# Kernel optimization log

Hardware: AMD Instinct MI355X
Metric: run time of the kernel (lower is better)

## Reference

```python
import jax, jax.numpy as jnp
import numpy as np

N_NODES = 50000
N_EDGES = 800000
N_REL = 3
N_GRAPHS = 500
EMB = 128
IN_DIM = EMB * 3
HID = 256
N_CLASS = 10
N_SHAPE, N_COLOR, MAX_POS = 8, 8, 128


def rgcn_layer(h, src, dst, etype, W, root, b):
    """PyG RGCNConv with default aggr='mean':
    out[v] = sum_r mean_{(j->v) in E_r} h[j] @ W[r] + h[v] @ root + b
    Aggregate raw features per (dst, relation) bucket, then apply relation matmuls.
    """
    N, R = h.shape[0], W.shape[0]
    seg = dst * R + etype  # combined (node, relation) segment id
    sums = jax.ops.segment_sum(h[src], seg, num_segments=N * R)          # (N*R, d)
    cnt = jax.ops.segment_sum(jnp.ones(seg.shape, h.dtype), seg, num_segments=N * R)
    mean = (sums / jnp.maximum(cnt, 1.0)[:, None]).reshape(N, R, -1)     # (N, R, d)
    return jnp.einsum('nrd,rdh->nh', mean, W) + h @ root + b


def setup_inputs() -> dict:
    key = jax.random.key(0)
    ks = jax.random.split(key, 20)
    f32 = jnp.float32
    inp = {
        's': jax.random.randint(ks[0], (N_NODES,), 0, N_SHAPE),
        'c': jax.random.randint(ks[1], (N_NODES,), 0, N_COLOR),
        'p': jax.random.randint(ks[2], (N_NODES,), 0, MAX_POS),
        'edge_index': jax.random.randint(ks[3], (2, N_EDGES), 0, N_NODES),
        'edge_type': jax.random.randint(ks[4], (N_EDGES,), 0, N_REL),
        'batch': jnp.sort(jax.random.randint(ks[5], (N_NODES,), 0, N_GRAPHS)),
        'shape_emb': jax.random.normal(ks[6], (N_SHAPE, EMB), f32),
        'color_emb': jax.random.normal(ks[7], (N_COLOR, EMB), f32),
        'pos_emb': jax.random.normal(ks[8], (MAX_POS, EMB), f32),
        'W1': jax.random.normal(ks[9], (N_REL, IN_DIM, HID), f32) / np.sqrt(IN_DIM),
        'root1': jax.random.normal(ks[10], (IN_DIM, HID), f32) / np.sqrt(IN_DIM),
        'b1': jnp.zeros((HID,), f32),
        'W2': jax.random.normal(ks[11], (N_REL, HID, HID), f32) / np.sqrt(HID),
        'root2': jax.random.normal(ks[12], (HID, HID), f32) / np.sqrt(HID),
        'b2': jnp.zeros((HID,), f32),
        'lin_w': jax.random.normal(ks[13], (HID, N_CLASS), f32) / np.sqrt(HID),
        'lin_b': jnp.zeros((N_CLASS,), f32),
    }
    return inp


def reference(s, c, p, edge_index, edge_type, batch,
              shape_emb, color_emb, pos_emb,
              W1, root1, b1, W2, root2, b2, lin_w, lin_b):
    src, dst = edge_index[0], edge_index[1]
    h = jnp.concatenate([shape_emb[s], color_emb[c], pos_emb[p]], axis=-1)  # (N, 3*emb)
    h = jax.nn.relu(rgcn_layer(h, src, dst, edge_type, W1, root1, b1))
    h = jax.nn.relu(rgcn_layer(h, src, dst, edge_type, W2, root2, b2))
    # global_mean_pool over graphs
    gsum = jax.ops.segment_sum(h, batch, num_segments=N_GRAPHS)
    gcnt = jax.ops.segment_sum(jnp.ones((h.shape[0],), h.dtype), batch, num_segments=N_GRAPHS)
    pooled = gsum / jnp.maximum(gcnt, 1.0)[:, None]
    return pooled @ lin_w + lin_b
```

## Files before the change

kernel.cpp:

```cpp
#include <hip/hip_runtime.h>
#include <hip/hip_bf16.h>

#define NN 50000
#define NE 800000
#define NR 3
#define NG 500
#define NB (NN * NR)
#define NCLS 10
#define NCMB 8192
#define CHUNK 2048
#define NBLK ((NB + CHUNK - 1) / CHUNK)

#define P1_COMBO   196
#define P1_ZCNT    586
#define P1_ZPOOL   502
#define P1_TAB     576
#define P1_WF      1024
#define P1_TOTAL   (P1_COMBO + P1_ZCNT + P1_ZPOOL + P1_TAB + P1_WF)
#define P2_CNT     3125
#define P2_COMB    (4 * NCMB)
#define P2_TOTAL   (P2_CNT + P2_COMB)

typedef __hip_bfloat16 bf16;
typedef __attribute__((ext_vector_type(8))) short short8;
typedef __attribute__((ext_vector_type(4))) float floatx4;

static __device__ __forceinline__ float b2f(bf16 x) { return __bfloat162float(x); }
static __device__ __forceinline__ bf16  f2b(float x) { return __float2bfloat16(x); }
static __device__ __forceinline__ float bs2f(short x) {
    return __bfloat162float(*reinterpret_cast<const bf16*>(&x));
}
static __device__ __forceinline__ short f2bs(float x) {
    bf16 b = __float2bfloat16(x);
    return *reinterpret_cast<const short*>(&b);
}

__global__ __launch_bounds__(256) void prep1(const int* __restrict__ s,
                                             const int* __restrict__ c,
                                             const int* __restrict__ p,
                                             const float* __restrict__ se,
                                             const float* __restrict__ ce,
                                             const float* __restrict__ pe,
                                             const float* __restrict__ W1,
                                             const float* __restrict__ root1,
                                             const float* __restrict__ W2,
                                             const float* __restrict__ root2,
                                             int* __restrict__ combo,
                                             unsigned* __restrict__ cnt,
                                             unsigned* __restrict__ poolz,
                                             float* __restrict__ tab,
                                             bf16* __restrict__ Wf) {
    int b = blockIdx.x, t = threadIdx.x;
    if (b < P1_COMBO) {
        int n = b * 256 + t;
        if (n < NN) combo[n] = (s[n] << 10) | (c[n] << 7) | p[n];
        return;
    }
    b -= P1_COMBO;
    if (b < P1_ZCNT) {
        int i = b * 256 + t;
        if (i < NB) cnt[i] = 0u;
        return;
    }
    b -= P1_ZCNT;
    if (b < P1_ZPOOL) {
        int i = b * 256 + t;
        if (i < NG * 256 + NG) poolz[i] = 0u;
        return;
    }
    b -= P1_ZPOOL;
    if (b < P1_TAB) {
        int r = b / 144, row = b % 144;
        const float* A; int segk;
        if (row < 8)       { A = se + row * 128;        segk = 0; }
        else if (row < 16) { A = ce + (row - 8) * 128;  segk = 128; }
        else               { A = pe + (row - 16) * 128; segk = 256; }
        const float* W = (r < 3) ? (W1 + (size_t)r * 384 * 256) : root1;
        float acc = 0.f;
        for (int k = 0; k < 128; ++k)
            acc += A[k] * W[(size_t)(segk + k) * 256 + t];
        tab[((size_t)r * 144 + row) * 256 + t] = acc;
        return;
    }
    b -= P1_TAB;
    {
        int idx = b * 256 + t;
        int j     = idx & 7;
        int lane  = (idx >> 3) & 63;
        int ni    = (idx >> 9) & 3;
        int chunk = (idx >> 11) & 31;
        int colblk = idx >> 16;
        int col = colblk * 64 + ni * 16 + (lane & 15);
        int k   = chunk * 32 + (lane >> 4) * 8 + j;
        float v = (k < 768) ? W2[((size_t)(k >> 8) * 256 + (k & 255)) * 256 + col]
                            : root2[(size_t)(k - 768) * 256 + col];
        Wf[idx] = f2b(v);
    }
}

__global__ __launch_bounds__(256) void prep2(const int* __restrict__ ei,
                                             const int* __restrict__ et,
                                             int* __restrict__ cnt,
                                             const float* __restrict__ tab,
                                             const float* __restrict__ b1,
                                             bf16* __restrict__ comb) {
    int b = blockIdx.x, t = threadIdx.x;
    if (b < P2_CNT) {
        int e = b * 256 + t;
        if (e < NE) atomicAdd(&cnt[ei[NE + e] * NR + et[e]], 1);
        return;
    }
    b -= P2_CNT;
    {
        int r = b >> 13, cmb = b & (NCMB - 1);
        int si = cmb >> 10, ci = (cmb >> 7) & 7, pi = cmb & 127;
        const float* tr = tab + (size_t)r * 144 * 256;
        float v = tr[si * 256 + t] + tr[(8 + ci) * 256 + t] + tr[(16 + pi) * 256 + t];
        if (r == 3) v += b1[t];
        comb[(size_t)b * 256 + t] = f2b(v);
    }
}

__global__ __launch_bounds__(256) void scan_block_sums(const int* __restrict__ cnt,
                                                       int* __restrict__ bsum) {
    __shared__ int sm[256];
    int b = blockIdx.x, t = threadIdx.x;
    int base = b * CHUNK + t * 8, s = 0;
#pragma unroll
    for (int j = 0; j < 8; ++j) { int i = base + j; if (i < NB) s += cnt[i]; }
    sm[t] = s; __syncthreads();
    for (int st = 128; st; st >>= 1) { if (t < st) sm[t] += sm[t + st]; __syncthreads(); }
    if (!t) bsum[b] = sm[0];
}

__global__ __launch_bounds__(256) void scan_write(const int* __restrict__ cnt,
                                                  const int* __restrict__ bsum,
                                                  int* __restrict__ off,
                                                  int* __restrict__ cursor) {
    int b = blockIdx.x, t = threadIdx.x;
    int bbase = 0;
    for (int i = 0; i < b; ++i) bbase += bsum[i];
    if (b == 0 && t == 0) {
        int tot = 0;
        for (int i = 0; i < NBLK; ++i) tot += bsum[i];
        off[NB] = tot;
    }
    int base = b * CHUNK + t * 8;
    int v[8], ts = 0;
#pragma unroll
    for (int j = 0; j < 8; ++j) { int i = base + j; v[j] = (i < NB) ? cnt[i] : 0; ts += v[j]; }
    int lane = t & 63, wv = t >> 6;
    int incl = ts;
    for (int d = 1; d < 64; d <<= 1) {
        int o = __shfl_up(incl, d, 64);
        if (lane >= d) incl += o;
    }
    __shared__ int wsum[4];
    if (lane == 63) wsum[wv] = incl;
    __syncthreads();
    int wbase = 0;
    for (int w = 0; w < wv; ++w) wbase += wsum[w];
    int run = bbase + wbase + incl - ts;
#pragma unroll
    for (int j = 0; j < 8; ++j) {
        int i = base + j;
        if (i < NB) { off[i] = run; cursor[i] = run; }
        run += v[j];
    }
}

__global__ __launch_bounds__(256) void scatter_edges(const int* __restrict__ ei,
                                                     const int* __restrict__ et,
                                                     const int* __restrict__ combo,
                                                     int* __restrict__ cursor,
                                                     int* __restrict__ eidx,
                                                     int* __restrict__ ecmb) {
    int e = blockIdx.x * 256 + threadIdx.x;
    if (e >= NE) return;
    int b = ei[NE + e] * NR + et[e];
    int pos = atomicAdd(&cursor[b], 1);
    int s = ei[e];
    eidx[pos] = s;
    ecmb[pos] = combo[s];
}

__global__ __launch_bounds__(256) void l1_fused(const int* __restrict__ off,
                                                const int* __restrict__ ecmb,
                                                const int* __restrict__ combo,
                                                const bf16* __restrict__ comb,
                                                bf16* __restrict__ h1) {
    int wave = threadIdx.x >> 6, lane = threadIdx.x & 63;
    int dst = blockIdx.x * 4 + wave;
    if (dst >= NN) return;
    int half = lane >> 5, li8 = (lane & 31) * 8;
    float acc[8];
    if (half == 0) {
        int cmbD = combo[dst];
        short8 rv = *(const short8*)(comb + ((size_t)(3 * NCMB) + cmbD) * 256 + li8);
#pragma unroll
        for (int i = 0; i < 8; ++i) acc[i] = bs2f(rv[i]);
    } else {
#pragma unroll
        for (int i = 0; i < 8; ++i) acc[i] = 0.f;
    }
    for (int r = 0; r < NR; ++r) {
        int lo = off[dst * NR + r], hi = off[dst * NR + r + 1];
        if (hi <= lo) continue;
        const bf16* cr = comb + (size_t)r * NCMB * 256;
        float s[8] = {};
        int j = lo;
        for (; j + 8 <= hi; j += 8) {
            int c0 = ecmb[j + half],     c1 = ecmb[j + 2 + half];
            int c2 = ecmb[j + 4 + half], c3 = ecmb[j + 6 + half];
            short8 v0 = *(const short8*)(cr + (size_t)c0 * 256 + li8);
            short8 v1 = *(const short8*)(cr + (size_t)c1 * 256 + li8);
            short8 v2 = *(const short8*)(cr + (size_t)c2 * 256 + li8);
            short8 v3 = *(const short8*)(cr + (size_t)c3 * 256 + li8);
#pragma unroll
            for (int i = 0; i < 8; ++i)
                s[i] += (bs2f(v0[i]) + bs2f(v1[i])) + (bs2f(v2[i]) + bs2f(v3[i]));
        }
        for (; j + 2 <= hi; j += 2) {
            int c0 = ecmb[j + half];
            short8 v0 = *(const short8*)(cr + (size_t)c0 * 256 + li8);
#pragma unroll
            for (int i = 0; i < 8; ++i) s[i] += bs2f(v0[i]);
        }
        if (j < hi && half == 0) {
            short8 v0 = *(const short8*)(cr + (size_t)ecmb[j] * 256 + li8);
#pragma unroll
            for (int i = 0; i < 8; ++i) s[i] += bs2f(v0[i]);
        }
        float inv = 1.0f / (float)(hi - lo);
#pragma unroll
        for (int i = 0; i < 8; ++i) {
            float tot = s[i] + __shfl_xor(s[i], 32);
            if (half == 0) acc[i] += tot * inv;
        }
    }
    if (half == 0) {
        short8 o;
#pragma unroll
        for (int i = 0; i < 8; ++i) o[i] = f2bs(fmaxf(acc[i], 0.f));
        *(short8*)(h1 + (size_t)dst * 256 + li8) = o;
    }
}

__global__ __launch_bounds__(256) void agg_all(const int* __restrict__ off,
                                               const int* __restrict__ eidx,
                                               const bf16* __restrict__ h1,
                                               bf16* __restrict__ hagg) {
    int wave = threadIdx.x >> 6, lane = threadIdx.x & 63;
    int dst = blockIdx.x * 4 + wave;
    if (dst >= NN) return;
    int half = lane >> 5, li8 = (lane & 31) * 8;
    for (int r = 0; r < NR; ++r) {
        int lo = off[dst * NR + r], hi = off[dst * NR + r + 1];
        float s[8] = {};
        int j = lo;
        for (; j + 8 <= hi; j += 8) {
            int e0 = eidx[j + half],     e1 = eidx[j + 2 + half];
            int e2 = eidx[j + 4 + half], e3 = eidx[j + 6 + half];
            short8 v0 = *(const short8*)(h1 + (size_t)e0 * 256 + li8);
            short8 v1 = *(const short8*)(h1 + (size_t)e1 * 256 + li8);
            short8 v2 = *(const short8*)(h1 + (size_t)e2 * 256 + li8);
            short8 v3 = *(const short8*)(h1 + (size_t)e3 * 256 + li8);
#pragma unroll
            for (int i = 0; i < 8; ++i)
                s[i] += (bs2f(v0[i]) + bs2f(v1[i])) + (bs2f(v2[i]) + bs2f(v3[i]));
        }
        for (; j + 2 <= hi; j += 2) {
            int e0 = eidx[j + half];
            short8 v0 = *(const short8*)(h1 + (size_t)e0 * 256 + li8);
#pragma unroll
            for (int i = 0; i < 8; ++i) s[i] += bs2f(v0[i]);
        }
        if (j < hi && half == 0) {
            short8 v0 = *(const short8*)(h1 + (size_t)eidx[j] * 256 + li8);
#pragma unroll
            for (int i = 0; i < 8; ++i) s[i] += bs2f(v0[i]);
        }
        float inv = (hi > lo) ? 1.0f / (float)(hi - lo) : 0.f;
        short8 o;
#pragma unroll
        for (int i = 0; i < 8; ++i) {
            float tot = s[i] + __shfl_xor(s[i], 32);
            o[i] = f2bs(tot * inv);
        }
        if (half == 0)
            *(short8*)(hagg + (size_t)dst * 768 + r * 256 + li8) = o;
    }
}

__global__ __launch_bounds__(256) void gemm_cat(const bf16* __restrict__ hagg,
                                                const bf16* __restrict__ h1,
                                                const bf16* __restrict__ Wf,
                                                const float* __restrict__ bias,
                                                const int* __restrict__ batch,
                                                float* __restrict__ pool,
                                                float* __restrict__ gcnt) {
    __shared__ short lds[4][2][32 * 40];
    const int t = threadIdx.x;
    const int wave = t >> 6, lane = t & 63;
    const int quad = lane >> 4, l16 = lane & 15;
    const int row0 = blockIdx.x * 32;
    const int colblk = wave;
    const int rsub = lane >> 2;
    const int ksub = (lane & 3) * 8;
    short* A0 = lds[wave][0];
    short* A1 = lds[wave][1];

    const int r0 = min(row0 + rsub, NN - 1);
    const int r1 = min(row0 + 16 + rsub, NN - 1);
    const bf16* gA0 = hagg + (size_t)r0 * 768 + ksub;
    const bf16* gA1 = hagg + (size_t)r1 * 768 + ksub;
    const bf16* gH0 = h1 + (size_t)r0 * 256 + ksub;
    const bf16* gH1 = h1 + (size_t)r1 * 256 + ksub;
    const short8* bbase = (const short8*)Wf + (size_t)colblk * 32 * 4 * 64 + lane;

    auto loadA2 = [&](int k0, short8& a0, short8& a1) {
        if (k0 < 768) { a0 = *(const short8*)(gA0 + k0); a1 = *(const short8*)(gA1 + k0); }
        else          { a0 = *(const short8*)(gH0 + k0 - 768); a1 = *(const short8*)(gH1 + k0 - 768); }
    };
    auto loadB = [&](int chunk, short8* bf4) {
        const short8* bp = bbase + (size_t)chunk * 4 * 64;
#pragma unroll
        for (int ni = 0; ni < 4; ++ni) bf4[ni] = bp[ni * 64];
    };

    floatx4 acc[2][4] = {};
    short8 aE0, aE1, bE[4];
    short8 aO0, aO1, bO[4];
    loadA2(0, aE0, aE1);  loadB(0, bE);
    loadA2(32, aO0, aO1); loadB(1, bO);

#pragma unroll
    for (int i = 0; i < 32; i += 2) {
        *(short8*)&A0[rsub * 40 + ksub] = aE0;
        *(short8*)&A0[(16 + rsub) * 40 + ksub] = aE1;
        {
            short8 af0 = *(const short8*)&A0[l16 * 40 + quad * 8];
            short8 af1 = *(const short8*)&A0[(16 + l16) * 40 + quad * 8];
#pragma unroll
            for (int ni = 0; ni < 4; ++ni) {
                acc[0][ni] = __builtin_amdgcn_mfma_f32_16x16x32_bf16(af0, bE[ni], acc[0][ni], 0, 0, 0);
                acc[1][ni] = __builtin_amdgcn_mfma_f32_16x16x32_bf16(af1, bE[ni], acc[1][ni], 0, 0, 0);
            }
        }
        if (i + 2 < 32) { loadA2((i + 2) * 32, aE0, aE1); loadB(i + 2, bE); }
        *(short8*)&A1[rsub * 40 + ksub] = aO0;
        *(short8*)&A1[(16 + rsub) * 40 + ksub] = aO1;
        {
            short8 af0 = *(const short8*)&A1[l16 * 40 + quad * 8];
            short8 af1 = *(const short8*)&A1[(16 + l16) * 40 + quad * 8];
#pragma unroll
            for (int ni = 0; ni < 4; ++ni) {
                acc[0][ni] = __builtin_amdgcn_mfma_f32_16x16x32_bf16(af0, bO[ni], acc[0][ni], 0, 0, 0);
                acc[1][ni] = __builtin_amdgcn_mfma_f32_16x16x32_bf16(af1, bO[ni], acc[1][ni], 0, 0, 0);
            }
        }
        if (i + 3 < 32) { loadA2((i + 3) * 32, aO0, aO1); loadB(i + 3, bO); }
    }

    __syncthreads();
    short* st = &lds[0][0][0];
#pragma unroll
    for (int mi = 0; mi < 2; ++mi) {
#pragma unroll
        for (int ni = 0; ni < 4; ++ni) {
            int n = colblk * 64 + ni * 16 + l16;
            float bn = bias[n];
#pragma unroll
            for (int ii = 0; ii < 4; ++ii) {
                int lrow = mi * 16 + quad * 4 + ii;
                float v = (row0 + lrow < NN) ? fmaxf(acc[mi][ni][ii] + bn, 0.f) : 0.f;
                st[lrow * 260 + n] = f2bs(v);
            }
        }
    }
    __syncthreads();
    int nrows = NN - row0; if (nrows > 32) nrows = 32;
    int curg = batch[row0];
    float a = 0.f, cntf = 0.f;
    for (int rr = 0; rr < nrows; ++rr) {
        int g = batch[row0 + rr];
        if (g != curg) {
            atomicAdd(&pool[(size_t)curg * 256 + t], a);
            if (t == 0) atomicAdd(&gcnt[curg], cntf);
            a = 0.f; cntf = 0.f; curg = g;
        }
        a += bs2f(st[rr * 260 + t]);
        cntf += 1.f;
    }
    atomicAdd(&pool[(size_t)curg * 256 + t], a);
    if (t == 0) atomicAdd(&gcnt[curg], cntf);
}

__global__ __launch_bounds__(256) void final_head(const float* __restrict__ pool,
                                                  const float* __restrict__ gcnt,
                                                  const float* __restrict__ lin_w,
                                                  const float* __restrict__ lin_b,
                                                  float* __restrict__ out) {
    __shared__ float sm[256];
    int g = blockIdx.x, t = threadIdx.x;
    float inv = 1.0f / fmaxf(gcnt[g], 1.0f);
    sm[t] = pool[(size_t)g * 256 + t] * inv;
    __syncthreads();
    if (t < NCLS) {
        float s = lin_b[t];
        for (int d = 0; d < 256; ++d) s += sm[d] * lin_w[d * NCLS + t];
        out[g * NCLS + t] = s;
    }
}

extern "C" void kernel_launch(void* const* d_in, const int* in_sizes, int n_in,
                              void* d_out, int out_size, void* d_ws, size_t ws_size,
                              hipStream_t stream) {
    const int*   s_idx = (const int*)d_in[0];
    const int*   c_idx = (const int*)d_in[1];
    const int*   p_idx = (const int*)d_in[2];
    const int*   ei    = (const int*)d_in[3];
    const int*   et    = (const int*)d_in[4];
    const int*   batch = (const int*)d_in[5];
    const float* se    = (const float*)d_in[6];
    const float* ce    = (const float*)d_in[7];
    const float* pe    = (const float*)d_in[8];
    const float* W1    = (const float*)d_in[9];
    const float* root1 = (const float*)d_in[10];
    const float* b1    = (const float*)d_in[11];
    const float* W2    = (const float*)d_in[12];
    const float* root2 = (const float*)d_in[13];
    const float* b2    = (const float*)d_in[14];
    const float* lin_w = (const float*)d_in[15];
    const float* lin_b = (const float*)d_in[16];
    float* out = (float*)d_out;

    char* w = (char*)d_ws;
    size_t o = 0;
    auto alloc = [&](size_t bytes) -> void* {
        o = (o + 15) & ~(size_t)15;
        void* ptr = w + o;
        o += bytes;
        return ptr;
    };
    bf16*  hagg   = (bf16*) alloc((size_t)NN * 768 * 2);
    bf16*  h1     = (bf16*) alloc((size_t)NN * 256 * 2);
    bf16*  comb   = (bf16*) alloc((size_t)4 * NCMB * 256 * 2);
    int*   combo  = (int*)  alloc((size_t)NN * 4);
    int*   eidx   = (int*)  alloc((size_t)NE * 4);
    int*   ecmb   = (int*)  alloc((size_t)NE * 4);
    int*   cnt    = (int*)  alloc((size_t)NB * 4);
    int*   off    = (int*)  alloc((size_t)(NB + 1) * 4);
    int*   cursor = (int*)  alloc((size_t)NB * 4);
    int*   bsum   = (int*)  alloc((size_t)NBLK * 4);
    float* tab    = (float*)alloc((size_t)4 * 144 * 256 * 4);
    bf16*  Wf     = (bf16*) alloc((size_t)256 * 1024 * 2);
    float* pool   = (float*)alloc((size_t)NG * 256 * 4);
    float* gcnt  = (float*)alloc((size_t)NG * 4);
    (void)ws_size;

    prep1<<<P1_TOTAL, 256, 0, stream>>>(s_idx, c_idx, p_idx, se, ce, pe,
                                        W1, root1, W2, root2,
                                        combo, (unsigned*)cnt, (unsigned*)pool, tab, Wf);
    prep2<<<P2_TOTAL, 256, 0, stream>>>(ei, et, cnt, tab, b1, comb);
    scan_block_sums<<<NBLK, 256, 0, stream>>>(cnt, bsum);
    scan_write<<<NBLK, 256, 0, stream>>>(cnt, bsum, off, cursor);
    scatter_edges<<<(NE + 255) / 256, 256, 0, stream>>>(ei, et, combo, cursor, eidx, ecmb);
    l1_fused<<<(NN + 3) / 4, 256, 0, stream>>>(off, ecmb, combo, comb, h1);
    agg_all<<<(NN + 3) / 4, 256, 0, stream>>>(off, eidx, h1, hagg);
    gemm_cat<<<(NN + 31) / 32, 256, 0, stream>>>(hagg, h1, Wf, b2, batch, pool, gcnt);
    final_head<<<NG, 256, 0, stream>>>(pool, gcnt, lin_w, lin_b, out);
}
```

Baseline: 395.0 us.

## Interleave three relation gathers per node and pack edge source/combo into int2

The two gather kernels now walk all three relation buckets of a destination node in one masked loop, so loads from each relation are in flight together instead of serialised per relation. Tail handling uses predicated loads with zero masks rather than separate remainder loops. The scatter step writes the source index and combo id as one int2, replacing two separate arrays. This adds wasted masked loads when bucket sizes are uneven, and each kernel now reads 8-byte entries where it used only 4 bytes.

```diff
diff --git a/kernel.cpp b/kernel.cpp
--- a/kernel.cpp
+++ b/kernel.cpp
@@ -173,19 +173,17 @@
                                                      const int* __restrict__ et,
                                                      const int* __restrict__ combo,
                                                      int* __restrict__ cursor,
-                                                     int* __restrict__ eidx,
-                                                     int* __restrict__ ecmb) {
+                                                     int2* __restrict__ esc) {
     int e = blockIdx.x * 256 + threadIdx.x;
     if (e >= NE) return;
     int b = ei[NE + e] * NR + et[e];
     int pos = atomicAdd(&cursor[b], 1);
     int s = ei[e];
-    eidx[pos] = s;
-    ecmb[pos] = combo[s];
+    esc[pos] = make_int2(s, combo[s]);
 }
 
 __global__ __launch_bounds__(256) void l1_fused(const int* __restrict__ off,
-                                                const int* __restrict__ ecmb,
+                                                const int2* __restrict__ esc,
                                                 const int* __restrict__ combo,
                                                 const bf16* __restrict__ comb,
                                                 bf16* __restrict__ h1) {
@@ -193,102 +191,106 @@
     int dst = blockIdx.x * 4 + wave;
     if (dst >= NN) return;
     int half = lane >> 5, li8 = (lane & 31) * 8;
-    float acc[8];
-    if (half == 0) {
-        int cmbD = combo[dst];
-        short8 rv = *(const short8*)(comb + ((size_t)(3 * NCMB) + cmbD) * 256 + li8);
-#pragma unroll
-        for (int i = 0; i < 8; ++i) acc[i] = bs2f(rv[i]);
-    } else {
-#pragma unroll
-        for (int i = 0; i < 8; ++i) acc[i] = 0.f;
-    }
-    for (int r = 0; r < NR; ++r) {
-        int lo = off[dst * NR + r], hi = off[dst * NR + r + 1];
-        if (hi <= lo) continue;
-        const bf16* cr = comb + (size_t)r * NCMB * 256;
-        float s[8] = {};
-        int j = lo;
-        for (; j + 8 <= hi; j += 8) {
-            int c0 = ecmb[j + half],     c1 = ecmb[j + 2 + half];
-            int c2 = ecmb[j + 4 + half], c3 = ecmb[j + 6 + half];
-            short8 v0 = *(const short8*)(cr + (size_t)c0 * 256 + li8);
-            short8 v1 = *(const short8*)(cr + (size_t)c1 * 256 + li8);
-            short8 v2 = *(const short8*)(cr + (size_t)c2 * 256 + li8);
-            short8 v3 = *(const short8*)(cr + (size_t)c3 * 256 + li8);
-#pragma unroll
-            for (int i = 0; i < 8; ++i)
-                s[i] += (bs2f(v0[i]) + bs2f(v1[i])) + (bs2f(v2[i]) + bs2f(v3[i]));
-        }
-        for (; j + 2 <= hi; j += 2) {
-            int c0 = ecmb[j + half];
-            short8 v0 = *(const short8*)(cr + (size_t)c0 * 256 + li8);
-#pragma unroll
-            for (int i = 0; i < 8; ++i) s[i] += bs2f(v0[i]);
-        }
-        if (j < hi && half == 0) {
-            short8 v0 = *(const short8*)(cr + (size_t)ecmb[j] * 256 + li8);
-#pragma unroll
-            for (int i = 0; i < 8; ++i) s[i] += bs2f(v0[i]);
-        }
-        float inv = 1.0f / (float)(hi - lo);
-#pragma unroll
-        for (int i = 0; i < 8; ++i) {
-            float tot = s[i] + __shfl_xor(s[i], 32);
-            if (half == 0) acc[i] += tot * inv;
-        }
-    }
-    if (half == 0) {
-        short8 o;
-#pragma unroll
-        for (int i = 0; i < 8; ++i) o[i] = f2bs(fmaxf(acc[i], 0.f));
+    int o0 = off[dst * NR],     o1 = off[dst * NR + 1],
+        o2 = off[dst * NR + 2], o3 = off[dst * NR + 3];
+    short8 rootv = {};
+    if (half == 0)
+        rootv = *(const short8*)(comb + ((size_t)(3 * NCMB) + combo[dst]) * 256 + li8);
+    const bf16* c0 = comb;
+    const bf16* c1 = comb + (size_t)NCMB * 256;
+    const bf16* c2 = comb + (size_t)2 * NCMB * 256;
+    float s0[8] = {}, s1[8] = {}, s2[8] = {};
+    int n = max((o1 - o0 + 1) >> 1, max((o2 - o1 + 1) >> 1, (o3 - o2 + 1) >> 1));
+    for (int k = 0; k < n; k += 2) {
+#pragma unroll
+        for (int kk = 0; kk < 2; ++kk) {
+            int i0 = o0 + 2 * (k + kk) + half;
+            int i1 = o1 + 2 * (k + kk) + half;
+            int i2 = o2 + 2 * (k + kk) + half;
+            bool g0 = i0 < o1, g1 = i1 < o2, g2 = i2 < o3;
+            int2 e0 = esc[g0 ? i0 : 0];
+            int2 e1 = esc[g1 ? i1 : 0];
+            int2 e2 = esc[g2 ? i2 : 0];
+            short8 v0 = *(const short8*)(c0 + (size_t)(g0 ? e0.y : 0) * 256 + li8);
+            short8 v1 = *(const short8*)(c1 + (size_t)(g1 ? e1.y : 0) * 256 + li8);
+            short8 v2 = *(const short8*)(c2 + (size_t)(g2 ? e2.y : 0) * 256 + li8);
+            float m0 = g0 ? 1.f : 0.f, m1 = g1 ? 1.f : 0.f, m2 = g2 ? 1.f : 0.f;
+#pragma unroll
+            for (int i = 0; i < 8; ++i) {
+                s0[i] += bs2f(v0[i]) * m0;
+                s1[i] += bs2f(v1[i]) * m1;
+                s2[i] += bs2f(v2[i]) * m2;
+            }
+        }
+    }
+    float inv0 = (o1 > o0) ? 1.f / (float)(o1 - o0) : 0.f;
+    float inv1 = (o2 > o1) ? 1.f / (float)(o2 - o1) : 0.f;
+    float inv2 = (o3 > o2) ? 1.f / (float)(o3 - o2) : 0.f;
+    short8 o;
+#pragma unroll
+    for (int i = 0; i < 8; ++i) {
+        float t0 = s0[i] + __shfl_xor(s0[i], 32);
+        float t1 = s1[i] + __shfl_xor(s1[i], 32);
+        float t2 = s2[i] + __shfl_xor(s2[i], 32);
+        float a = bs2f(rootv[i]) + t0 * inv0 + t1 * inv1 + t2 * inv2;
+        o[i] = f2bs(fmaxf(a, 0.f));
+    }
+    if (half == 0)
         *(short8*)(h1 + (size_t)dst * 256 + li8) = o;
-    }
 }
 
 __global__ __launch_bounds__(256) void agg_all(const int* __restrict__ off,
-                                               const int* __restrict__ eidx,
+                                               const int2* __restrict__ esc,
                                                const bf16* __restrict__ h1,
                                                bf16* __restrict__ hagg) {
     int wave = threadIdx.x >> 6, lane = threadIdx.x & 63;
     int dst = blockIdx.x * 4 + wave;
     if (dst >= NN) return;
     int half = lane >> 5, li8 = (lane & 31) * 8;
-    for (int r = 0; r < NR; ++r) {
-        int lo = off[dst * NR + r], hi = off[dst * NR + r + 1];
-        float s[8] = {};
-        int j = lo;
-        for (; j + 8 <= hi; j += 8) {
-            int e0 = eidx[j + half],     e1 = eidx[j + 2 + half];
-            int e2 = eidx[j + 4 + half], e3 = eidx[j + 6 + half];
-            short8 v0 = *(const short8*)(h1 + (size_t)e0 * 256 + li8);
-            short8 v1 = *(const short8*)(h1 + (size_t)e1 * 256 + li8);
-            short8 v2 = *(const short8*)(h1 + (size_t)e2 * 256 + li8);
-            short8 v3 = *(const short8*)(h1 + (size_t)e3 * 256 + li8);
-#pragma unroll
-            for (int i = 0; i < 8; ++i)
-                s[i] += (bs2f(v0[i]) + bs2f(v1[i])) + (bs2f(v2[i]) + bs2f(v3[i]));
-        }
-        for (; j + 2 <= hi; j += 2) {
-            int e0 = eidx[j + half];
-            short8 v0 = *(const short8*)(h1 + (size_t)e0 * 256 + li8);
-#pragma unroll
-            for (int i = 0; i < 8; ++i) s[i] += bs2f(v0[i]);
-        }
-        if (j < hi && half == 0) {
-            short8 v0 = *(const short8*)(h1 + (size_t)eidx[j] * 256 + li8);
-#pragma unroll
-            for (int i = 0; i < 8; ++i) s[i] += bs2f(v0[i]);
-        }
-        float inv = (hi > lo) ? 1.0f / (float)(hi - lo) : 0.f;
-        short8 o;
-#pragma unroll
-        for (int i = 0; i < 8; ++i) {
-            float tot = s[i] + __shfl_xor(s[i], 32);
-            o[i] = f2bs(tot * inv);
-        }
-        if (half == 0)
-            *(short8*)(hagg + (size_t)dst * 768 + r * 256 + li8) = o;
+    int o0 = off[dst * NR],     o1 = off[dst * NR + 1],
+        o2 = off[dst * NR + 2], o3 = off[dst * NR + 3];
+    float s0[8] = {}, s1[8] = {}, s2[8] = {};
+    int n = max((o1 - o0 + 1) >> 1, max((o2 - o1 + 1) >> 1, (o3 - o2 + 1) >> 1));
+    for (int k = 0; k < n; k += 2) {
+#pragma unroll
+        for (int kk = 0; kk < 2; ++kk) {
+            int i0 = o0 + 2 * (k + kk) + half;
+            int i1 = o1 + 2 * (k + kk) + half;
+            int i2 = o2 + 2 * (k + kk) + half;
+            bool g0 = i0 < o1, g1 = i1 < o2, g2 = i2 < o3;
+            int2 e0 = esc[g0 ? i0 : 0];
+            int2 e1 = esc[g1 ? i1 : 0];
+            int2 e2 = esc[g2 ? i2 : 0];
+            short8 v0 = *(const short8*)(h1 + (size_t)(g0 ? e0.x : 0) * 256 + li8);
+            short8 v1 = *(const short8*)(h1 + (size_t)(g1 ? e1.x : 0) * 256 + li8);
+            short8 v2 = *(const short8*)(h1 + (size_t)(g2 ? e2.x : 0) * 256 + li8);
+            float m0 = g0 ? 1.f : 0.f, m1 = g1 ? 1.f : 0.f, m2 = g2 ? 1.f : 0.f;
+#pragma unroll
+            for (int i = 0; i < 8; ++i) {
+                s0[i] += bs2f(v0[i]) * m0;
+                s1[i] += bs2f(v1[i]) * m1;
+                s2[i] += bs2f(v2[i]) * m2;
+            }
+        }
+    }
+    float inv0 = (o1 > o0) ? 1.f / (float)(o1 - o0) : 0.f;
+    float inv1 = (o2 > o1) ? 1.f / (float)(o2 - o1) : 0.f;
+    float inv2 = (o3 > o2) ? 1.f / (float)(o3 - o2) : 0.f;
+    short8 w0, w1, w2;
+#pragma unroll
+    for (int i = 0; i < 8; ++i) {
+        float t0 = s0[i] + __shfl_xor(s0[i], 32);
+        float t1 = s1[i] + __shfl_xor(s1[i], 32);
+        float t2 = s2[i] + __shfl_xor(s2[i], 32);
+        w0[i] = f2bs(t0 * inv0);
+        w1[i] = f2bs(t1 * inv1);
+        w2[i] = f2bs(t2 * inv2);
+    }
+    if (half == 0) {
+        bf16* hd = hagg + (size_t)dst * 768 + li8;
+        *(short8*)(hd)       = w0;
+        *(short8*)(hd + 256) = w1;
+        *(short8*)(hd + 512) = w2;
     }
 }
 
@@ -447,8 +449,7 @@
     bf16*  h1     = (bf16*) alloc((size_t)NN * 256 * 2);
     bf16*  comb   = (bf16*) alloc((size_t)4 * NCMB * 256 * 2);
     int*   combo  = (int*)  alloc((size_t)NN * 4);
-    int*   eidx   = (int*)  alloc((size_t)NE * 4);
-    int*   ecmb   = (int*)  alloc((size_t)NE * 4);
+    int2*  esc    = (int2*) alloc((size_t)NE * 8);
     int*   cnt    = (int*)  alloc((size_t)NB * 4);
     int*   off    = (int*)  alloc((size_t)(NB + 1) * 4);
     int*   cursor = (int*)  alloc((size_t)NB * 4);
@@ -465,9 +466,9 @@
     prep2<<<P2_TOTAL, 256, 0, stream>>>(ei, et, cnt, tab, b1, comb);
     scan_block_sums<<<NBLK, 256, 0, stream>>>(cnt, bsum);
     scan_write<<<NBLK, 256, 0, stream>>>(cnt, bsum, off, cursor);
-    scatter_edges<<<(NE + 255) / 256, 256, 0, stream>>>(ei, et, combo, cursor, eidx, ecmb);
-    l1_fused<<<(NN + 3) / 4, 256, 0, stream>>>(off, ecmb, combo, comb, h1);
-    agg_all<<<(NN + 3) / 4, 256, 0, stream>>>(off, eidx, h1, hagg);
+    scatter_edges<<<(NE + 255) / 256, 256, 0, stream>>>(ei, et, combo, cursor, esc);
+    l1_fused<<<(NN + 3) / 4, 256, 0, stream>>>(off, esc, combo, comb, h1);
+    agg_all<<<(NN + 3) / 4, 256, 0, stream>>>(off, esc, h1, hagg);
     gemm_cat<<<(NN + 31) / 32, 256, 0, stream>>>(hagg, h1, Wf, b2, batch, pool, gcnt);
     final_head<<<NG, 256, 0, stream>>>(pool, gcnt, lin_w, lin_b, out);
 }
```

Result: faster. 383.3 us (-2.9%).

## Fuse layer-2 aggregation into GEMM and pack edge src/combo into one word

Applied to the files above, without the earlier changes.

The layer-2 neighbor aggregation now runs inside the GEMM kernel. Each block gathers the mean-aggregated rows for its 32 nodes straight into a swizzled LDS tile, so the 150 MB-scale hagg intermediate is never written or re-read from global memory. The per-edge source index and combo index are packed into one 32-bit word, which halves the edge-list traffic. Layer 1 now walks all three relations in a single merged loop with per-edge weights. The trade-off is a large 64 KB LDS tile per block, which lowers occupancy, and the aggregation phase is serialized ahead of the MFMA phase within each block.

```diff
diff --git a/kernel.cpp b/kernel.cpp
--- a/kernel.cpp
+++ b/kernel.cpp
@@ -173,19 +173,17 @@
                                                      const int* __restrict__ et,
                                                      const int* __restrict__ combo,
                                                      int* __restrict__ cursor,
-                                                     int* __restrict__ eidx,
-                                                     int* __restrict__ ecmb) {
+                                                     unsigned* __restrict__ esc) {
     int e = blockIdx.x * 256 + threadIdx.x;
     if (e >= NE) return;
     int b = ei[NE + e] * NR + et[e];
     int pos = atomicAdd(&cursor[b], 1);
     int s = ei[e];
-    eidx[pos] = s;
-    ecmb[pos] = combo[s];
+    esc[pos] = ((unsigned)s << 13) | (unsigned)combo[s];
 }
 
 __global__ __launch_bounds__(256) void l1_fused(const int* __restrict__ off,
-                                                const int* __restrict__ ecmb,
+                                                const unsigned* __restrict__ esc,
                                                 const int* __restrict__ combo,
                                                 const bf16* __restrict__ comb,
                                                 bf16* __restrict__ h1) {
@@ -193,177 +191,178 @@
     int dst = blockIdx.x * 4 + wave;
     if (dst >= NN) return;
     int half = lane >> 5, li8 = (lane & 31) * 8;
-    float acc[8];
-    if (half == 0) {
-        int cmbD = combo[dst];
-        short8 rv = *(const short8*)(comb + ((size_t)(3 * NCMB) + cmbD) * 256 + li8);
-#pragma unroll
-        for (int i = 0; i < 8; ++i) acc[i] = bs2f(rv[i]);
-    } else {
-#pragma unroll
-        for (int i = 0; i < 8; ++i) acc[i] = 0.f;
-    }
-    for (int r = 0; r < NR; ++r) {
-        int lo = off[dst * NR + r], hi = off[dst * NR + r + 1];
-        if (hi <= lo) continue;
-        const bf16* cr = comb + (size_t)r * NCMB * 256;
-        float s[8] = {};
-        int j = lo;
-        for (; j + 8 <= hi; j += 8) {
-            int c0 = ecmb[j + half],     c1 = ecmb[j + 2 + half];
-            int c2 = ecmb[j + 4 + half], c3 = ecmb[j + 6 + half];
-            short8 v0 = *(const short8*)(cr + (size_t)c0 * 256 + li8);
-            short8 v1 = *(const short8*)(cr + (size_t)c1 * 256 + li8);
-            short8 v2 = *(const short8*)(cr + (size_t)c2 * 256 + li8);
-            short8 v3 = *(const short8*)(cr + (size_t)c3 * 256 + li8);
-#pragma unroll
-            for (int i = 0; i < 8; ++i)
-                s[i] += (bs2f(v0[i]) + bs2f(v1[i])) + (bs2f(v2[i]) + bs2f(v3[i]));
-        }
-        for (; j + 2 <= hi; j += 2) {
-            int c0 = ecmb[j + half];
-            short8 v0 = *(const short8*)(cr + (size_t)c0 * 256 + li8);
-#pragma unroll
-            for (int i = 0; i < 8; ++i) s[i] += bs2f(v0[i]);
-        }
-        if (j < hi && half == 0) {
-            short8 v0 = *(const short8*)(cr + (size_t)ecmb[j] * 256 + li8);
-#pragma unroll
-            for (int i = 0; i < 8; ++i) s[i] += bs2f(v0[i]);
-        }
-        float inv = 1.0f / (float)(hi - lo);
-#pragma unroll
-        for (int i = 0; i < 8; ++i) {
-            float tot = s[i] + __shfl_xor(s[i], 32);
-            if (half == 0) acc[i] += tot * inv;
-        }
-    }
-    if (half == 0) {
-        short8 o;
-#pragma unroll
-        for (int i = 0; i < 8; ++i) o[i] = f2bs(fmaxf(acc[i], 0.f));
+    int b0 = dst * NR;
+    int o0 = off[b0], o1 = off[b0 + 1], o2 = off[b0 + 2], o3 = off[b0 + 3];
+    float inv0 = (o1 > o0) ? 1.f / (float)(o1 - o0) : 0.f;
+    float inv1 = (o2 > o1) ? 1.f / (float)(o2 - o1) : 0.f;
+    float inv2 = (o3 > o2) ? 1.f / (float)(o3 - o2) : 0.f;
+    short8 rootv = {};
+    if (half == 0)
+        rootv = *(const short8*)(comb + ((size_t)(3 * NCMB) + combo[dst]) * 256 + li8);
+    float s[8] = {};
+    int j = o0;
+    for (; j + 8 <= o3; j += 8) {
+        int k0 = j + half, k1 = j + 2 + half, k2 = j + 4 + half, k3 = j + 6 + half;
+        unsigned e0 = esc[k0], e1 = esc[k1], e2 = esc[k2], e3 = esc[k3];
+        int ro0 = ((k0 >= o1) ? NCMB : 0) + ((k0 >= o2) ? NCMB : 0);
+        int ro1 = ((k1 >= o1) ? NCMB : 0) + ((k1 >= o2) ? NCMB : 0);
+        int ro2 = ((k2 >= o1) ? NCMB : 0) + ((k2 >= o2) ? NCMB : 0);
+        int ro3 = ((k3 >= o1) ? NCMB : 0) + ((k3 >= o2) ? NCMB : 0);
+        short8 v0 = *(const short8*)(comb + (size_t)(ro0 + (e0 & (NCMB - 1))) * 256 + li8);
+        short8 v1 = *(const short8*)(comb + (size_t)(ro1 + (e1 & (NCMB - 1))) * 256 + li8);
+        short8 v2 = *(const short8*)(comb + (size_t)(ro2 + (e2 & (NCMB - 1))) * 256 + li8);
+        short8 v3 = *(const short8*)(comb + (size_t)(ro3 + (e3 & (NCMB - 1))) * 256 + li8);
+        float w0 = (k0 >= o2) ? inv2 : ((k0 >= o1) ? inv1 : inv0);
+        float w1 = (k1 >= o2) ? inv2 : ((k1 >= o1) ? inv1 : inv0);
+        float w2 = (k2 >= o2) ? inv2 : ((k2 >= o1) ? inv1 : inv0);
+        float w3 = (k3 >= o2) ? inv2 : ((k3 >= o1) ? inv1 : inv0);
+#pragma unroll
+        for (int i = 0; i < 8; ++i)
+            s[i] += bs2f(v0[i]) * w0 + bs2f(v1[i]) * w1
+                  + bs2f(v2[i]) * w2 + bs2f(v3[i]) * w3;
+    }
+    for (; j + 2 <= o3; j += 2) {
+        int k0 = j + half;
+        unsigned e0 = esc[k0];
+        int ro0 = ((k0 >= o1) ? NCMB : 0) + ((k0 >= o2) ? NCMB : 0);
+        short8 v0 = *(const short8*)(comb + (size_t)(ro0 + (e0 & (NCMB - 1))) * 256 + li8);
+        float w0 = (k0 >= o2) ? inv2 : ((k0 >= o1) ? inv1 : inv0);
+#pragma unroll
+        for (int i = 0; i < 8; ++i) s[i] += bs2f(v0[i]) * w0;
+    }
+    if (j < o3 && half == 0) {
+        int k0 = j;
+        unsigned e0 = esc[k0];
+        int ro0 = ((k0 >= o1) ? NCMB : 0) + ((k0 >= o2) ? NCMB : 0);
+        short8 v0 = *(const short8*)(comb + (size_t)(ro0 + (e0 & (NCMB - 1))) * 256 + li8);
+        float w0 = (k0 >= o2) ? inv2 : ((k0 >= o1) ? inv1 : inv0);
+#pragma unroll
+        for (int i = 0; i < 8; ++i) s[i] += bs2f(v0[i]) * w0;
+    }
+    short8 o;
+#pragma unroll
+    for (int i = 0; i < 8; ++i) {
+        float tot = s[i] + __shfl_xor(s[i], 32);
+        o[i] = f2bs(fmaxf(bs2f(rootv[i]) + tot, 0.f));
+    }
+    if (half == 0)
         *(short8*)(h1 + (size_t)dst * 256 + li8) = o;
-    }
-}
-
-__global__ __launch_bounds__(256) void agg_all(const int* __restrict__ off,
-                                               const int* __restrict__ eidx,
-                                               const bf16* __restrict__ h1,
-                                               bf16* __restrict__ hagg) {
-    int wave = threadIdx.x >> 6, lane = threadIdx.x & 63;
-    int dst = blockIdx.x * 4 + wave;
-    if (dst >= NN) return;
-    int half = lane >> 5, li8 = (lane & 31) * 8;
-    for (int r = 0; r < NR; ++r) {
-        int lo = off[dst * NR + r], hi = off[dst * NR + r + 1];
-        float s[8] = {};
-        int j = lo;
-        for (; j + 8 <= hi; j += 8) {
-            int e0 = eidx[j + half],     e1 = eidx[j + 2 + half];
-            int e2 = eidx[j + 4 + half], e3 = eidx[j + 6 + half];
-            short8 v0 = *(const short8*)(h1 + (size_t)e0 * 256 + li8);
-            short8 v1 = *(const short8*)(h1 + (size_t)e1 * 256 + li8);
-            short8 v2 = *(const short8*)(h1 + (size_t)e2 * 256 + li8);
-            short8 v3 = *(const short8*)(h1 + (size_t)e3 * 256 + li8);
-#pragma unroll
-            for (int i = 0; i < 8; ++i)
-                s[i] += (bs2f(v0[i]) + bs2f(v1[i])) + (bs2f(v2[i]) + bs2f(v3[i]));
-        }
-        for (; j + 2 <= hi; j += 2) {
-            int e0 = eidx[j + half];
-            short8 v0 = *(const short8*)(h1 + (size_t)e0 * 256 + li8);
-#pragma unroll
-            for (int i = 0; i < 8; ++i) s[i] += bs2f(v0[i]);
-        }
-        if (j < hi && half == 0) {
-            short8 v0 = *(const short8*)(h1 + (size_t)eidx[j] * 256 + li8);
-#pragma unroll
-            for (int i = 0; i < 8; ++i) s[i] += bs2f(v0[i]);
-        }
-        float inv = (hi > lo) ? 1.0f / (float)(hi - lo) : 0.f;
-        short8 o;
-#pragma unroll
-        for (int i = 0; i < 8; ++i) {
-            float tot = s[i] + __shfl_xor(s[i], 32);
-            o[i] = f2bs(tot * inv);
-        }
-        if (half == 0)
-            *(short8*)(hagg + (size_t)dst * 768 + r * 256 + li8) = o;
-    }
-}
-
-__global__ __launch_bounds__(256) void gemm_cat(const bf16* __restrict__ hagg,
+}
+
+__global__ __launch_bounds__(256) void l2_fused(const int* __restrict__ off,
+                                                const unsigned* __restrict__ esc,
                                                 const bf16* __restrict__ h1,
                                                 const bf16* __restrict__ Wf,
                                                 const float* __restrict__ bias,
                                                 const int* __restrict__ batch,
                                                 float* __restrict__ pool,
                                                 float* __restrict__ gcnt) {
-    __shared__ short lds[4][2][32 * 40];
+    __shared__ short A[32 * 1024];
     const int t = threadIdx.x;
     const int wave = t >> 6, lane = t & 63;
+    const int half = lane >> 5, li8 = (lane & 31) * 8;
+    const int row0 = blockIdx.x * 32;
+
+    for (int d = 0; d < 8; ++d) {
+        int dstrow = wave * 8 + d;
+        int dst = row0 + dstrow;
+        bool val = dst < NN;
+        int b0 = val ? dst * NR : 0;
+        int o0 = off[b0], o1 = off[b0 + 1], o2 = off[b0 + 2], o3 = off[b0 + 3];
+        if (!val) { o1 = o0; o2 = o0; o3 = o0; }
+        int lo = o0;
+#pragma unroll
+        for (int r = 0; r < NR; ++r) {
+            int hi = (r == 0) ? o1 : (r == 1) ? o2 : o3;
+            float s[8] = {};
+            int j = lo;
+            for (; j + 8 <= hi; j += 8) {
+                unsigned e0 = esc[j + half],     e1 = esc[j + 2 + half];
+                unsigned e2 = esc[j + 4 + half], e3 = esc[j + 6 + half];
+                short8 v0 = *(const short8*)(h1 + (size_t)(e0 >> 13) * 256 + li8);
+                short8 v1 = *(const short8*)(h1 + (size_t)(e1 >> 13) * 256 + li8);
+                short8 v2 = *(const short8*)(h1 + (size_t)(e2 >> 13) * 256 + li8);
+                short8 v3 = *(const short8*)(h1 + (size_t)(e3 >> 13) * 256 + li8);
+#pragma unroll
+                for (int i = 0; i < 8; ++i)
+                    s[i] += (bs2f(v0[i]) + bs2f(v1[i])) + (bs2f(v2[i]) + bs2f(v3[i]));
+            }
+            for (; j + 2 <= hi; j += 2) {
+                unsigned e0 = esc[j + half];
+                short8 v0 = *(const short8*)(h1 + (size_t)(e0 >> 13) * 256 + li8);
+#pragma unroll
+                for (int i = 0; i < 8; ++i) s[i] += bs2f(v0[i]);
+            }
+            if (j < hi && half == 0) {
+                unsigned e0 = esc[j];
+                short8 v0 = *(const short8*)(h1 + (size_t)(e0 >> 13) * 256 + li8);
+#pragma unroll
+                for (int i = 0; i < 8; ++i) s[i] += bs2f(v0[i]);
+            }
+            float inv = (hi > lo) ? 1.f / (float)(hi - lo) : 0.f;
+            short8 o;
+#pragma unroll
+            for (int i = 0; i < 8; ++i) {
+                float tot = s[i] + __shfl_xor(s[i], 32);
+                o[i] = f2bs(tot * inv);
+            }
+            if (half == 0) {
+                int colb = (r * 256 + li8) * 2;
+                *(short8*)((char*)A + dstrow * 2048 + (colb ^ ((dstrow & 7) << 4))) = o;
+            }
+            lo = hi;
+        }
+        if (half == 0) {
+            short8 hv = {};
+            if (val) hv = *(const short8*)(h1 + (size_t)dst * 256 + li8);
+            int colb = (768 + li8) * 2;
+            *(short8*)((char*)A + dstrow * 2048 + (colb ^ ((dstrow & 7) << 4))) = hv;
+        }
+    }
+    __syncthreads();
+
     const int quad = lane >> 4, l16 = lane & 15;
-    const int row0 = blockIdx.x * 32;
     const int colblk = wave;
-    const int rsub = lane >> 2;
-    const int ksub = (lane & 3) * 8;
-    short* A0 = lds[wave][0];
-    short* A1 = lds[wave][1];
-
-    const int r0 = min(row0 + rsub, NN - 1);
-    const int r1 = min(row0 + 16 + rsub, NN - 1);
-    const bf16* gA0 = hagg + (size_t)r0 * 768 + ksub;
-    const bf16* gA1 = hagg + (size_t)r1 * 768 + ksub;
-    const bf16* gH0 = h1 + (size_t)r0 * 256 + ksub;
-    const bf16* gH1 = h1 + (size_t)r1 * 256 + ksub;
     const short8* bbase = (const short8*)Wf + (size_t)colblk * 32 * 4 * 64 + lane;
-
-    auto loadA2 = [&](int k0, short8& a0, short8& a1) {
-        if (k0 < 768) { a0 = *(const short8*)(gA0 + k0); a1 = *(const short8*)(gA1 + k0); }
-        else          { a0 = *(const short8*)(gH0 + k0 - 768); a1 = *(const short8*)(gH1 + k0 - 768); }
-    };
     auto loadB = [&](int chunk, short8* bf4) {
         const short8* bp = bbase + (size_t)chunk * 4 * 64;
 #pragma unroll
         for (int ni = 0; ni < 4; ++ni) bf4[ni] = bp[ni * 64];
     };
+    auto ldA = [&](int row, int colE) -> short8 {
+        int byte = (colE * 2) ^ ((row & 7) << 4);
+        return *(const short8*)((const char*)A + row * 2048 + byte);
+    };
 
     floatx4 acc[2][4] = {};
-    short8 aE0, aE1, bE[4];
-    short8 aO0, aO1, bO[4];
-    loadA2(0, aE0, aE1);  loadB(0, bE);
-    loadA2(32, aO0, aO1); loadB(1, bO);
-
-#pragma unroll
-    for (int i = 0; i < 32; i += 2) {
-        *(short8*)&A0[rsub * 40 + ksub] = aE0;
-        *(short8*)&A0[(16 + rsub) * 40 + ksub] = aE1;
+    short8 bE[4], bO[4];
+    loadB(0, bE); loadB(1, bO);
+#pragma unroll
+    for (int ch = 0; ch < 32; ch += 2) {
         {
-            short8 af0 = *(const short8*)&A0[l16 * 40 + quad * 8];
-            short8 af1 = *(const short8*)&A0[(16 + l16) * 40 + quad * 8];
+            short8 af0 = ldA(l16, ch * 32 + quad * 8);
+            short8 af1 = ldA(16 + l16, ch * 32 + quad * 8);
 #pragma unroll
             for (int ni = 0; ni < 4; ++ni) {
                 acc[0][ni] = __builtin_amdgcn_mfma_f32_16x16x32_bf16(af0, bE[ni], acc[0][ni], 0, 0, 0);
                 acc[1][ni] = __builtin_amdgcn_mfma_f32_16x16x32_bf16(af1, bE[ni], acc[1][ni], 0, 0, 0);
             }
         }
-        if (i + 2 < 32) { loadA2((i + 2) * 32, aE0, aE1); loadB(i + 2, bE); }
-        *(short8*)&A1[rsub * 40 + ksub] = aO0;
-        *(short8*)&A1[(16 + rsub) * 40 + ksub] = aO1;
+        if (ch + 2 < 32) loadB(ch + 2, bE);
         {
-            short8 af0 = *(const short8*)&A1[l16 * 40 + quad * 8];
-            short8 af1 = *(const short8*)&A1[(16 + l16) * 40 + quad * 8];
+            short8 af0 = ldA(l16, (ch + 1) * 32 + quad * 8);
+            short8 af1 = ldA(16 + l16, (ch + 1) * 32 + quad * 8);
 #pragma unroll
             for (int ni = 0; ni < 4; ++ni) {
                 acc[0][ni] = __builtin_amdgcn_mfma_f32_16x16x32_bf16(af0, bO[ni], acc[0][ni], 0, 0, 0);
                 acc[1][ni] = __builtin_amdgcn_mfma_f32_16x16x32_bf16(af1, bO[ni], acc[1][ni], 0, 0, 0);
             }
         }
-        if (i + 3 < 32) { loadA2((i + 3) * 32, aO0, aO1); loadB(i + 3, bO); }
+        if (ch + 3 < 32) loadB(ch + 3, bO);
     }
 
     __syncthreads();
-    short* st = &lds[0][0][0];
+    short* st = A;
 #pragma unroll
     for (int mi = 0; mi < 2; ++mi) {
 #pragma unroll
@@ -443,20 +442,18 @@
         o += bytes;
         return ptr;
     };
-    bf16*  hagg   = (bf16*) alloc((size_t)NN * 768 * 2);
-    bf16*  h1     = (bf16*) alloc((size_t)NN * 256 * 2);
-    bf16*  comb   = (bf16*) alloc((size_t)4 * NCMB * 256 * 2);
-    int*   combo  = (int*)  alloc((size_t)NN * 4);
-    int*   eidx   = (int*)  alloc((size_t)NE * 4);
-    int*   ecmb   = (int*)  alloc((size_t)NE * 4);
-    int*   cnt    = (int*)  alloc((size_t)NB * 4);
-    int*   off    = (int*)  alloc((size_t)(NB + 1) * 4);
-    int*   cursor = (int*)  alloc((size_t)NB * 4);
-    int*   bsum   = (int*)  alloc((size_t)NBLK * 4);
-    float* tab    = (float*)alloc((size_t)4 * 144 * 256 * 4);
-    bf16*  Wf     = (bf16*) alloc((size_t)256 * 1024 * 2);
-    float* pool   = (float*)alloc((size_t)NG * 256 * 4);
-    float* gcnt  = (float*)alloc((size_t)NG * 4);
+    bf16*     h1     = (bf16*)    alloc((size_t)NN * 256 * 2);
+    bf16*     comb   = (bf16*)    alloc((size_t)4 * NCMB * 256 * 2);
+    int*      combo  = (int*)     alloc((size_t)NN * 4);
+    unsigned* esc    = (unsigned*)alloc((size_t)NE * 4);
+    int*      cnt    = (int*)     alloc((size_t)NB * 4);
+    int*      off    = (int*)     alloc((size_t)(NB + 1) * 4);
+    int*      cursor = (int*)     alloc((size_t)NB * 4);
+    int*      bsum   = (int*)     alloc((size_t)NBLK * 4);
+    float*    tab    = (float*)   alloc((size_t)4 * 144 * 256 * 4);
+    bf16*     Wf     = (bf16*)    alloc((size_t)256 * 1024 * 2);
+    float*    pool   = (float*)   alloc((size_t)NG * 256 * 4);
+    float*    gcnt   = (float*)   alloc((size_t)NG * 4);
     (void)ws_size;
 
     prep1<<<P1_TOTAL, 256, 0, stream>>>(s_idx, c_idx, p_idx, se, ce, pe,
@@ -465,9 +462,8 @@
     prep2<<<P2_TOTAL, 256, 0, stream>>>(ei, et, cnt, tab, b1, comb);
     scan_block_sums<<<NBLK, 256, 0, stream>>>(cnt, bsum);
     scan_write<<<NBLK, 256, 0, stream>>>(cnt, bsum, off, cursor);
-    scatter_edges<<<(NE + 255) / 256, 256, 0, stream>>>(ei, et, combo, cursor, eidx, ecmb);
-    l1_fused<<<(NN + 3) / 4, 256, 0, stream>>>(off, ecmb, combo, comb, h1);
-    agg_all<<<(NN + 3) / 4, 256, 0, stream>>>(off, eidx, h1, hagg);
-    gemm_cat<<<(NN + 31) / 32, 256, 0, stream>>>(hagg, h1, Wf, b2, batch, pool, gcnt);
+    scatter_edges<<<(NE + 255) / 256, 256, 0, stream>>>(ei, et, combo, cursor, esc);
+    l1_fused<<<(NN + 3) / 4, 256, 0, stream>>>(off, esc, combo, comb, h1);
+    l2_fused<<<(NN + 31) / 32, 256, 0, stream>>>(off, esc, h1, Wf, b2, batch, pool, gcnt);
     final_head<<<NG, 256, 0, stream>>>(pool, gcnt, lin_w, lin_b, out);
 }
```

Result: slower. 497.6 us (+26.0%).
